# Kernel tuning notes

Hardware: AMD Instinct MI355X
Metric: run time of the kernel (lower is better)

Reference implementation:

```python
import jax, jax.numpy as jnp
import numpy as np

N_U, N_I, E, D = 100000, 50000, 1600000, 128


def setup_inputs() -> dict:
    key = jax.random.key(0)
    ks = jax.random.split(key, 24)
    inp = {
        "x_user": jax.random.normal(ks[0], (N_U, D), jnp.float32),
        "x_item": jax.random.normal(ks[1], (N_I, D), jnp.float32),
        "follows_src": jax.random.randint(ks[2], (E,), 0, N_U, jnp.int32),
        "follows_dst": jax.random.randint(ks[3], (E,), 0, N_U, jnp.int32),
        "rates_src": jax.random.randint(ks[4], (E,), 0, N_U, jnp.int32),
        "rates_dst": jax.random.randint(ks[5], (E,), 0, N_I, jnp.int32),
        "rev_src": jax.random.randint(ks[6], (E,), 0, N_I, jnp.int32),
        "rev_dst": jax.random.randint(ks[7], (E,), 0, N_U, jnp.int32),
    }
    scale = 1.0 / np.sqrt(D)
    wnames = ["W1_follows", "W1_rates", "W1_rev", "W2_follows", "W2_rates", "W2_rev"]
    for i, name in enumerate(wnames):
        inp[name] = jax.random.normal(ks[8 + i], (D, D), jnp.float32) * scale
    bnames = ["b1_follows", "b1_rates", "b1_rev", "b2_follows", "b2_rates", "b2_rev"]
    for i, name in enumerate(bnames):
        inp[name] = jax.random.normal(ks[14 + i], (D,), jnp.float32) * 0.02
    return inp


def _gcn_conv(x_src, src, dst, n_src, n_dst, W, b):
    """Degree-normalized GCN conv on a (possibly bipartite) relation."""
    ones = jnp.ones(src.shape, x_src.dtype)
    deg_s = jax.ops.segment_sum(ones, src, num_segments=n_src)
    deg_d = jax.ops.segment_sum(ones, dst, num_segments=n_dst)
    inv_s = jnp.where(deg_s > 0, 1.0 / jnp.sqrt(deg_s), 0.0)
    inv_d = jnp.where(deg_d > 0, 1.0 / jnp.sqrt(deg_d), 0.0)
    h = x_src @ W                                   # [n_src, out]
    norm = inv_s[src] * inv_d[dst]                  # [E]
    msg = h[src] * norm[:, None]                    # gather + scale
    out = jax.ops.segment_sum(msg, dst, num_segments=n_dst)  # scatter-add
    return out + b


def reference(x_user, x_item, follows_src, follows_dst, rates_src, rates_dst,
              rev_src, rev_dst, W1_follows, b1_follows, W1_rates, b1_rates,
              W1_rev, b1_rev, W2_follows, b2_follows, W2_rates, b2_rates,
              W2_rev, b2_rev):
    # Layer 1: HeteroConv with aggr='mean' over relations sharing dst type
    u = (_gcn_conv(x_user, follows_src, follows_dst, N_U, N_U, W1_follows, b1_follows)
         + _gcn_conv(x_item, rev_src, rev_dst, N_I, N_U, W1_rev, b1_rev)) * 0.5
    it = _gcn_conv(x_user, rates_src, rates_dst, N_U, N_I, W1_rates, b1_rates)
    u = jax.nn.relu(u)
    it = jax.nn.relu(it)
    # Layer 2 (final layer: no relu)
    u2 = (_gcn_conv(u, follows_src, follows_dst, N_U, N_U, W2_follows, b2_follows)
          + _gcn_conv(it, rev_src, rev_dst, N_I, N_U, W2_rev, b2_rev)) * 0.5
    i2 = _gcn_conv(u, rates_src, rates_dst, N_U, N_I, W2_rates, b2_rates)
    # concat node-type outputs into a single array: [N_U + N_I, D]
    return jnp.concatenate([u2, i2], axis=0)
```

## Files before the change

kernel.cpp:

```cpp
#include <hip/hip_runtime.h>
#include <math.h>

static constexpr int NU    = 100000;
static constexpr int NI    = 50000;
static constexpr int NEDGE = 1600000;
static constexpr int DIM   = 128;

__global__ void count_deg_kernel(const int* __restrict__ src, const int* __restrict__ dst,
                                 int* __restrict__ deg_s, int* __restrict__ deg_d, int n) {
  int stride = gridDim.x * blockDim.x;
  for (int i = blockIdx.x * blockDim.x + threadIdx.x; i < n; i += stride) {
    atomicAdd(&deg_s[src[i]], 1);
    atomicAdd(&deg_d[dst[i]], 1);
  }
}

__global__ void inv_sqrt_kernel(int* __restrict__ p, int n) {
  int i = blockIdx.x * blockDim.x + threadIdx.x;
  if (i < n) {
    int v = p[i];
    float f = (v > 0) ? (1.0f / sqrtf((float)v)) : 0.0f;
    p[i] = __float_as_int(f);
  }
}

__global__ __launch_bounds__(1024) void scan_kernel(const int* __restrict__ deg, int n,
                                                    int* __restrict__ rp) {
  __shared__ int wsum[16];
  __shared__ int carry_s;
  const int tid = threadIdx.x, lane = tid & 63, wid = tid >> 6;
  if (tid == 0) carry_s = 0;
  __syncthreads();
  for (int base = 0; base < n; base += 4096) {
    int i0 = base + tid * 4;
    int v0 = 0, v1 = 0, v2 = 0, v3 = 0;
    if (i0 + 3 < n) {
      int4 t = *(const int4*)(deg + i0);
      v0 = t.x; v1 = t.y; v2 = t.z; v3 = t.w;
    } else {
      if (i0     < n) v0 = deg[i0];
      if (i0 + 1 < n) v1 = deg[i0 + 1];
      if (i0 + 2 < n) v2 = deg[i0 + 2];
    }
    int s0 = v0, s1 = s0 + v1, s2 = s1 + v2, s3 = s2 + v3;
    int tot = s3;
    int x = tot;
#pragma unroll
    for (int d2 = 1; d2 < 64; d2 <<= 1) { int y = __shfl_up(x, d2); if (lane >= d2) x += y; }
    if (lane == 63) wsum[wid] = x;
    __syncthreads();
    if (wid == 0) {
      int s = (lane < 16) ? wsum[lane] : 0;
#pragma unroll
      for (int d2 = 1; d2 < 16; d2 <<= 1) { int y = __shfl_up(s, d2); if (lane >= d2) s += y; }
      if (lane < 16) wsum[lane] = s;
    }
    __syncthreads();
    int carry = carry_s;
    int woff = (wid > 0) ? wsum[wid - 1] : 0;
    int base_excl = carry + woff + (x - tot);
    if (i0     < n) rp[i0]     = base_excl;
    if (i0 + 1 < n) rp[i0 + 1] = base_excl + s0;
    if (i0 + 2 < n) rp[i0 + 2] = base_excl + s1;
    if (i0 + 3 < n) rp[i0 + 3] = base_excl + s2;
    __syncthreads();
    if (tid == 0) carry_s = carry + wsum[15];
    __syncthreads();
  }
  if (tid == 0) rp[n] = carry_s;
}

__global__ void fill_kernel(const int* __restrict__ src, const int* __restrict__ dst,
                            const int* __restrict__ rp, int* __restrict__ cnt,
                            int* __restrict__ csr, int n) {
  int stride = gridDim.x * blockDim.x;
  for (int i = blockIdx.x * blockDim.x + threadIdx.x; i < n; i += stride) {
    int d = dst[i];
    int p = atomicAdd(&cnt[d], 1);
    csr[rp[d] + p] = src[i];
  }
}

__global__ __launch_bounds__(256) void gemm128_kernel(const float* __restrict__ A,
                                                      const float* __restrict__ W,
                                                      float* __restrict__ C, int M) {
  __shared__ float As[16][132];
  __shared__ float Bs[16][128];
  const int tid = threadIdx.x;
  const int tx = tid & 15, ty = tid >> 4;
  const int row0 = blockIdx.x * 128;
  float acc[8][8];
#pragma unroll
  for (int r = 0; r < 8; ++r)
#pragma unroll
    for (int c = 0; c < 8; ++c) acc[r][c] = 0.f;

  for (int kk = 0; kk < DIM; kk += 16) {
#pragma unroll
    for (int p = 0; p < 2; ++p) {
      int r = (tid >> 2) + p * 64;
      int kc = (tid & 3) * 4;
      float4 a = make_float4(0.f, 0.f, 0.f, 0.f);
      int row = row0 + r;
      if (row < M) a = *(const float4*)(A + (size_t)row * DIM + kk + kc);
      As[kc + 0][r] = a.x; As[kc + 1][r] = a.y; As[kc + 2][r] = a.z; As[kc + 3][r] = a.w;
    }
    {
      const float4* srcp = (const float4*)(W + kk * DIM);
      float4* dstp = (float4*)(&Bs[0][0]);
      dstp[tid]       = srcp[tid];
      dstp[tid + 256] = srcp[tid + 256];
    }
    __syncthreads();
#pragma unroll
    for (int k = 0; k < 16; ++k) {
      float a[8], b[8];
      *(float4*)&a[0] = *(const float4*)&As[k][ty * 8];
      *(float4*)&a[4] = *(const float4*)&As[k][ty * 8 + 4];
      *(float4*)&b[0] = *(const float4*)&Bs[k][tx * 8];
      *(float4*)&b[4] = *(const float4*)&Bs[k][tx * 8 + 4];
#pragma unroll
      for (int r = 0; r < 8; ++r)
#pragma unroll
        for (int c = 0; c < 8; ++c) acc[r][c] += a[r] * b[c];
    }
    __syncthreads();
  }
#pragma unroll
  for (int r = 0; r < 8; ++r) {
    int row = row0 + ty * 8 + r;
    if (row < M) {
      float4* cp = (float4*)(C + (size_t)row * DIM + tx * 8);
      cp[0] = make_float4(acc[r][0], acc[r][1], acc[r][2], acc[r][3]);
      cp[1] = make_float4(acc[r][4], acc[r][5], acc[r][6], acc[r][7]);
    }
  }
}

template <int MODE, bool RELU>
__global__ __launch_bounds__(256) void agg_kernel(const float* __restrict__ h,
                                                  const int* __restrict__ rp,
                                                  const int* __restrict__ csr,
                                                  const float* __restrict__ inv_s,
                                                  const float* __restrict__ inv_d,
                                                  float* __restrict__ out, int n_dst,
                                                  float scale,
                                                  const float* __restrict__ b1,
                                                  const float* __restrict__ b2) {
  const int lane = threadIdx.x & 63;
  const int row = blockIdx.x * (blockDim.x >> 6) + (threadIdx.x >> 6);
  if (row >= n_dst) return;
  const int e0 = rp[row], e1 = rp[row + 1];
  float ax = 0.f, ay = 0.f;
  for (int base = e0; base < e1; base += 64) {
    const int rem = e1 - base;
    const int m = rem < 64 ? rem : 64;
    int s_l = 0; float w_l = 0.f;
    if (lane < m) { s_l = csr[base + lane]; w_l = inv_s[s_l]; }
    int j = 0;
    for (; j + 3 < m; j += 4) {
      int s0 = __shfl(s_l, j), s1 = __shfl(s_l, j + 1), s2 = __shfl(s_l, j + 2), s3 = __shfl(s_l, j + 3);
      float w0 = __shfl(w_l, j), w1 = __shfl(w_l, j + 1), w2 = __shfl(w_l, j + 2), w3 = __shfl(w_l, j + 3);
      float2 v0 = ((const float2*)(h + (size_t)s0 * DIM))[lane];
      float2 v1 = ((const float2*)(h + (size_t)s1 * DIM))[lane];
      float2 v2 = ((const float2*)(h + (size_t)s2 * DIM))[lane];
      float2 v3 = ((const float2*)(h + (size_t)s3 * DIM))[lane];
      ax += w0 * v0.x + w1 * v1.x + w2 * v2.x + w3 * v3.x;
      ay += w0 * v0.y + w1 * v1.y + w2 * v2.y + w3 * v3.y;
    }
    for (; j < m; ++j) {
      int s0 = __shfl(s_l, j); float w0 = __shfl(w_l, j);
      float2 v0 = ((const float2*)(h + (size_t)s0 * DIM))[lane];
      ax += w0 * v0.x; ay += w0 * v0.y;
    }
  }
  const float invd = inv_d[row];
  float rx = ax * invd, ry = ay * invd;
  float2* op = (float2*)(out + (size_t)row * DIM);
  if (MODE == 0) {
    op[lane] = make_float2(rx, ry);
  } else {
    float bx = 0.f, by = 0.f;
    if (b1) { float2 b = ((const float2*)b1)[lane]; bx += b.x; by += b.y; }
    if (b2) { float2 b = ((const float2*)b2)[lane]; bx += b.x; by += b.y; }
    float px = 0.f, py = 0.f;
    if (MODE == 1) { float2 p = op[lane]; px = p.x; py = p.y; }
    float vx = scale * (px + rx + bx), vy = scale * (py + ry + by);
    if (RELU) { vx = fmaxf(vx, 0.f); vy = fmaxf(vy, 0.f); }
    op[lane] = make_float2(vx, vy);
  }
}

extern "C" void kernel_launch(void* const* d_in, const int* in_sizes, int n_in,
                              void* d_out, int out_size, void* d_ws, size_t ws_size,
                              hipStream_t stream) {
  const float* x_user = (const float*)d_in[0];
  const float* x_item = (const float*)d_in[1];
  const int* f_src = (const int*)d_in[2];
  const int* f_dst = (const int*)d_in[3];
  const int* r_src = (const int*)d_in[4];
  const int* r_dst = (const int*)d_in[5];
  const int* v_src = (const int*)d_in[6];
  const int* v_dst = (const int*)d_in[7];
  const float* W1f = (const float*)d_in[8];
  const float* W1r = (const float*)d_in[9];
  const float* W1v = (const float*)d_in[10];
  const float* W2f = (const float*)d_in[11];
  const float* W2r = (const float*)d_in[12];
  const float* W2v = (const float*)d_in[13];
  const float* b1f = (const float*)d_in[14];
  const float* b1r = (const float*)d_in[15];
  const float* b1v = (const float*)d_in[16];
  const float* b2f = (const float*)d_in[17];
  const float* b2r = (const float*)d_in[18];
  const float* b2v = (const float*)d_in[19];

  char* ws = (char*)d_ws;
  size_t off = 0;
  auto alloc = [&](size_t bytes) {
    size_t o = off;
    off = (off + bytes + 511) & ~(size_t)511;
    return o;
  };
  size_t o_deg = alloc(4ull * (4 * NU + 2 * NI));
  size_t o_rpf = alloc(4ull * (NU + 1));
  size_t o_rpr = alloc(4ull * (NI + 1));
  size_t o_rpv = alloc(4ull * (NU + 1));
  size_t o_cnt = alloc(4ull * (2 * NU + NI));
  size_t o_csf = alloc(4ull * NEDGE);
  size_t o_csr = alloc(4ull * NEDGE);
  size_t o_csv = alloc(4ull * NEDGE);
  size_t o_h   = alloc(4ull * NU * DIM);
  size_t o_u   = alloc(4ull * NU * DIM);
  size_t o_it  = alloc(4ull * NI * DIM);
  (void)ws_size; (void)in_sizes; (void)n_in; (void)out_size;

  int* deg    = (int*)(ws + o_deg);
  int* deg_fs = deg;
  int* deg_fd = deg + NU;
  int* deg_rs = deg + 2 * NU;
  int* deg_rd = deg + 3 * NU;
  int* deg_vs = deg + 3 * NU + NI;
  int* deg_vd = deg + 3 * NU + 2 * NI;

  int* rp_f = (int*)(ws + o_rpf);
  int* rp_r = (int*)(ws + o_rpr);
  int* rp_v = (int*)(ws + o_rpv);
  int* cnt   = (int*)(ws + o_cnt);
  int* cnt_f = cnt;
  int* cnt_r = cnt + NU;
  int* cnt_v = cnt + NU + NI;
  int* csr_f = (int*)(ws + o_csf);
  int* csr_r = (int*)(ws + o_csr);
  int* csr_v = (int*)(ws + o_csv);
  float* h  = (float*)(ws + o_h);
  float* u  = (float*)(ws + o_u);
  float* it = (float*)(ws + o_it);

  float* out_u = (float*)d_out;
  float* out_i = out_u + (size_t)NU * DIM;

  hipMemsetAsync(deg, 0, 4ull * (4 * NU + 2 * NI), stream);
  hipMemsetAsync(cnt, 0, 4ull * (2 * NU + NI), stream);

  count_deg_kernel<<<2048, 256, 0, stream>>>(f_src, f_dst, deg_fs, deg_fd, NEDGE);
  count_deg_kernel<<<2048, 256, 0, stream>>>(r_src, r_dst, deg_rs, deg_rd, NEDGE);
  count_deg_kernel<<<2048, 256, 0, stream>>>(v_src, v_dst, deg_vs, deg_vd, NEDGE);

  scan_kernel<<<1, 1024, 0, stream>>>(deg_fd, NU, rp_f);
  scan_kernel<<<1, 1024, 0, stream>>>(deg_rd, NI, rp_r);
  scan_kernel<<<1, 1024, 0, stream>>>(deg_vd, NU, rp_v);

  inv_sqrt_kernel<<<(4 * NU + 2 * NI + 255) / 256, 256, 0, stream>>>(deg, 4 * NU + 2 * NI);

  fill_kernel<<<2048, 256, 0, stream>>>(f_src, f_dst, rp_f, cnt_f, csr_f, NEDGE);
  fill_kernel<<<2048, 256, 0, stream>>>(r_src, r_dst, rp_r, cnt_r, csr_r, NEDGE);
  fill_kernel<<<2048, 256, 0, stream>>>(v_src, v_dst, rp_v, cnt_v, csr_v, NEDGE);

  const float* inv_fs = (const float*)deg_fs;
  const float* inv_fd = (const float*)deg_fd;
  const float* inv_rs = (const float*)deg_rs;
  const float* inv_rd = (const float*)deg_rd;
  const float* inv_vs = (const float*)deg_vs;
  const float* inv_vd = (const float*)deg_vd;

  gemm128_kernel<<<(NU + 127) / 128, 256, 0, stream>>>(x_user, W1f, h, NU);
  agg_kernel<0, false><<<(NU + 3) / 4, 256, 0, stream>>>(h, rp_f, csr_f, inv_fs, inv_fd,
                                                         u, NU, 1.0f, nullptr, nullptr);
  gemm128_kernel<<<(NI + 127) / 128, 256, 0, stream>>>(x_item, W1v, h, NI);
  agg_kernel<1, true><<<(NU + 3) / 4, 256, 0, stream>>>(h, rp_v, csr_v, inv_vs, inv_vd,
                                                        u, NU, 0.5f, b1f, b1v);
  gemm128_kernel<<<(NU + 127) / 128, 256, 0, stream>>>(x_user, W1r, h, NU);
  agg_kernel<2, true><<<(NI + 3) / 4, 256, 0, stream>>>(h, rp_r, csr_r, inv_rs, inv_rd,
                                                        it, NI, 1.0f, b1r, nullptr);

  gemm128_kernel<<<(NU + 127) / 128, 256, 0, stream>>>(u, W2f, h, NU);
  agg_kernel<0, false><<<(NU + 3) / 4, 256, 0, stream>>>(h, rp_f, csr_f, inv_fs, inv_fd,
                                                         out_u, NU, 1.0f, nullptr, nullptr);
  gemm128_kernel<<<(NI + 127) / 128, 256, 0, stream>>>(it, W2v, h, NI);
  agg_kernel<1, false><<<(NU + 3) / 4, 256, 0, stream>>>(h, rp_v, csr_v, inv_vs, inv_vd,
                                                         out_u, NU, 0.5f, b2f, b2v);
  gemm128_kernel<<<(NU + 127) / 128, 256, 0, stream>>>(u, W2r, h, NU);
  agg_kernel<2, false><<<(NI + 3) / 4, 256, 0, stream>>>(h, rp_r, csr_r, inv_rs, inv_rd,
                                                         out_i, NI, 1.0f, b2r, nullptr);
}
```

Baseline: 2.037 ms.

## Co-schedule independent graph build, GEMMs and aggregations in merged kernels

Degree counting now records each edge's atomic rank, so the CSR fill needs no second atomic counter pass or memset of counters. Independent work (degree counting plus the three layer-1 GEMMs, CSR fills plus the first aggregation, paired aggregations, layer-2 GEMMs plus aggregation) is packed into combined kernels using block-index ranges. This cuts launch count and lets independent stages run concurrently on the GPU. It uses separate h buffers per relation when the workspace is large enough, with a fallback sequential path that reuses buffers otherwise.

```diff
diff --git a/kernel.cpp b/kernel.cpp
--- a/kernel.cpp
+++ b/kernel.cpp
@@ -6,89 +6,57 @@
 static constexpr int NEDGE = 1600000;
 static constexpr int DIM   = 128;
 
-__global__ void count_deg_kernel(const int* __restrict__ src, const int* __restrict__ dst,
-                                 int* __restrict__ deg_s, int* __restrict__ deg_d, int n) {
-  int stride = gridDim.x * blockDim.x;
-  for (int i = blockIdx.x * blockDim.x + threadIdx.x; i < n; i += stride) {
-    atomicAdd(&deg_s[src[i]], 1);
-    atomicAdd(&deg_d[dst[i]], 1);
-  }
-}
-
-__global__ void inv_sqrt_kernel(int* __restrict__ p, int n) {
-  int i = blockIdx.x * blockDim.x + threadIdx.x;
-  if (i < n) {
-    int v = p[i];
-    float f = (v > 0) ? (1.0f / sqrtf((float)v)) : 0.0f;
-    p[i] = __float_as_int(f);
-  }
-}
-
-__global__ __launch_bounds__(1024) void scan_kernel(const int* __restrict__ deg, int n,
-                                                    int* __restrict__ rp) {
-  __shared__ int wsum[16];
-  __shared__ int carry_s;
-  const int tid = threadIdx.x, lane = tid & 63, wid = tid >> 6;
-  if (tid == 0) carry_s = 0;
-  __syncthreads();
-  for (int base = 0; base < n; base += 4096) {
-    int i0 = base + tid * 4;
-    int v0 = 0, v1 = 0, v2 = 0, v3 = 0;
-    if (i0 + 3 < n) {
-      int4 t = *(const int4*)(deg + i0);
-      v0 = t.x; v1 = t.y; v2 = t.z; v3 = t.w;
-    } else {
-      if (i0     < n) v0 = deg[i0];
-      if (i0 + 1 < n) v1 = deg[i0 + 1];
-      if (i0 + 2 < n) v2 = deg[i0 + 2];
-    }
-    int s0 = v0, s1 = s0 + v1, s2 = s1 + v2, s3 = s2 + v3;
-    int tot = s3;
-    int x = tot;
-#pragma unroll
-    for (int d2 = 1; d2 < 64; d2 <<= 1) { int y = __shfl_up(x, d2); if (lane >= d2) x += y; }
-    if (lane == 63) wsum[wid] = x;
-    __syncthreads();
-    if (wid == 0) {
-      int s = (lane < 16) ? wsum[lane] : 0;
-#pragma unroll
-      for (int d2 = 1; d2 < 16; d2 <<= 1) { int y = __shfl_up(s, d2); if (lane >= d2) s += y; }
-      if (lane < 16) wsum[lane] = s;
-    }
-    __syncthreads();
-    int carry = carry_s;
-    int woff = (wid > 0) ? wsum[wid - 1] : 0;
-    int base_excl = carry + woff + (x - tot);
-    if (i0     < n) rp[i0]     = base_excl;
-    if (i0 + 1 < n) rp[i0 + 1] = base_excl + s0;
-    if (i0 + 2 < n) rp[i0 + 2] = base_excl + s1;
-    if (i0 + 3 < n) rp[i0 + 3] = base_excl + s2;
-    __syncthreads();
-    if (tid == 0) carry_s = carry + wsum[15];
-    __syncthreads();
-  }
-  if (tid == 0) rp[n] = carry_s;
-}
-
-__global__ void fill_kernel(const int* __restrict__ src, const int* __restrict__ dst,
-                            const int* __restrict__ rp, int* __restrict__ cnt,
-                            int* __restrict__ csr, int n) {
-  int stride = gridDim.x * blockDim.x;
-  for (int i = blockIdx.x * blockDim.x + threadIdx.x; i < n; i += stride) {
-    int d = dst[i];
-    int p = atomicAdd(&cnt[d], 1);
-    csr[rp[d] + p] = src[i];
-  }
-}
-
-__global__ __launch_bounds__(256) void gemm128_kernel(const float* __restrict__ A,
-                                                      const float* __restrict__ W,
-                                                      float* __restrict__ C, int M) {
-  __shared__ float As[16][132];
-  __shared__ float Bs[16][128];
+static constexpr int CB  = 768;
+static constexpr int GF  = (NU + 127) / 128;
+static constexpr int GV  = (NI + 127) / 128;
+static constexpr int FB  = 512;
+static constexpr int AGU = (NU + 3) / 4;
+static constexpr int AGI = (NI + 3) / 4;
+
+__device__ __forceinline__ void count_rel(const int* __restrict__ src, const int* __restrict__ dst,
+                                          int* __restrict__ deg_s, int* __restrict__ deg_d,
+                                          int* __restrict__ rank, int blk, int nblk) {
+  const int nchunk = NEDGE / 4;
+  const int stride = nblk * 256;
+  for (int c = blk * 256 + threadIdx.x; c < nchunk; c += stride) {
+    int4 s = ((const int4*)src)[c];
+    int4 d = ((const int4*)dst)[c];
+    atomicAdd(&deg_s[s.x], 1);
+    atomicAdd(&deg_s[s.y], 1);
+    atomicAdd(&deg_s[s.z], 1);
+    atomicAdd(&deg_s[s.w], 1);
+    int4 r;
+    r.x = atomicAdd(&deg_d[d.x], 1);
+    r.y = atomicAdd(&deg_d[d.y], 1);
+    r.z = atomicAdd(&deg_d[d.z], 1);
+    r.w = atomicAdd(&deg_d[d.w], 1);
+    ((int4*)rank)[c] = r;
+  }
+}
+
+__device__ __forceinline__ void fill_rel(const int* __restrict__ src, const int* __restrict__ dst,
+                                         const int* __restrict__ rank, const int* __restrict__ rp,
+                                         int* __restrict__ csr, int blk, int nblk) {
+  const int nchunk = NEDGE / 4;
+  const int stride = nblk * 256;
+  for (int c = blk * 256 + threadIdx.x; c < nchunk; c += stride) {
+    int4 s = ((const int4*)src)[c];
+    int4 d = ((const int4*)dst)[c];
+    int4 r = ((const int4*)rank)[c];
+    csr[rp[d.x] + r.x] = s.x;
+    csr[rp[d.y] + r.y] = s.y;
+    csr[rp[d.z] + r.z] = s.z;
+    csr[rp[d.w] + r.w] = s.w;
+  }
+}
+
+__device__ __forceinline__ void gemm_body(const float* __restrict__ A, const float* __restrict__ W,
+                                          float* __restrict__ C, int M, int blk) {
+  static __shared__ float As[16][132];
+  static __shared__ float Bs[16][128];
   const int tid = threadIdx.x;
   const int tx = tid & 15, ty = tid >> 4;
-  const int row0 = blockIdx.x * 128;
+  const int row0 = blk * 128;
   float acc[8][8];
 #pragma unroll
   for (int r = 0; r < 8; ++r)
@@ -138,17 +106,13 @@
 }
 
 template <int MODE, bool RELU>
-__global__ __launch_bounds__(256) void agg_kernel(const float* __restrict__ h,
-                                                  const int* __restrict__ rp,
-                                                  const int* __restrict__ csr,
-                                                  const float* __restrict__ inv_s,
-                                                  const float* __restrict__ inv_d,
-                                                  float* __restrict__ out, int n_dst,
-                                                  float scale,
-                                                  const float* __restrict__ b1,
-                                                  const float* __restrict__ b2) {
+__device__ __forceinline__ void agg_rows(const float* __restrict__ h, const int* __restrict__ rp,
+                                         const int* __restrict__ csr, const float* __restrict__ inv_s,
+                                         const float* __restrict__ inv_d, float* __restrict__ out,
+                                         int n_dst, float scale, const float* __restrict__ b1,
+                                         const float* __restrict__ b2, int blk) {
   const int lane = threadIdx.x & 63;
-  const int row = blockIdx.x * (blockDim.x >> 6) + (threadIdx.x >> 6);
+  const int row = blk * 4 + (threadIdx.x >> 6);
   if (row >= n_dst) return;
   const int e0 = rp[row], e1 = rp[row + 1];
   float ax = 0.f, ay = 0.f;
@@ -189,6 +153,157 @@
     if (RELU) { vx = fmaxf(vx, 0.f); vy = fmaxf(vy, 0.f); }
     op[lane] = make_float2(vx, vy);
   }
+}
+
+__device__ void scan_body(const int* __restrict__ deg, int n, int* __restrict__ rp) {
+  static __shared__ int wsum[16];
+  static __shared__ int carry_s;
+  const int tid = threadIdx.x, lane = tid & 63, wid = tid >> 6;
+  if (tid == 0) carry_s = 0;
+  __syncthreads();
+  for (int base = 0; base < n; base += 4096) {
+    int i0 = base + tid * 4;
+    int v0 = 0, v1 = 0, v2 = 0, v3 = 0;
+    if (i0 + 3 < n) {
+      int4 t = *(const int4*)(deg + i0);
+      v0 = t.x; v1 = t.y; v2 = t.z; v3 = t.w;
+    } else {
+      if (i0     < n) v0 = deg[i0];
+      if (i0 + 1 < n) v1 = deg[i0 + 1];
+      if (i0 + 2 < n) v2 = deg[i0 + 2];
+    }
+    int s0 = v0, s1 = s0 + v1, s2 = s1 + v2, s3 = s2 + v3;
+    int tot = s3;
+    int x = tot;
+#pragma unroll
+    for (int d2 = 1; d2 < 64; d2 <<= 1) { int y = __shfl_up(x, d2); if (lane >= d2) x += y; }
+    if (lane == 63) wsum[wid] = x;
+    __syncthreads();
+    if (wid == 0) {
+      int s = (lane < 16) ? wsum[lane] : 0;
+#pragma unroll
+      for (int d2 = 1; d2 < 16; d2 <<= 1) { int y = __shfl_up(s, d2); if (lane >= d2) s += y; }
+      if (lane < 16) wsum[lane] = s;
+    }
+    __syncthreads();
+    int carry = carry_s;
+    int woff = (wid > 0) ? wsum[wid - 1] : 0;
+    int base_excl = carry + woff + (x - tot);
+    if (i0     < n) rp[i0]     = base_excl;
+    if (i0 + 1 < n) rp[i0 + 1] = base_excl + s0;
+    if (i0 + 2 < n) rp[i0 + 2] = base_excl + s1;
+    if (i0 + 3 < n) rp[i0 + 3] = base_excl + s2;
+    __syncthreads();
+    if (tid == 0) carry_s = carry + wsum[15];
+    __syncthreads();
+  }
+  if (tid == 0) rp[n] = carry_s;
+}
+
+
+__global__ __launch_bounds__(256) void k1_kernel(
+    const int* f_src, const int* f_dst, int* deg_fs, int* deg_fd, int* rank_f,
+    const int* r_src, const int* r_dst, int* deg_rs, int* deg_rd, int* rank_r,
+    const int* v_src, const int* v_dst, int* deg_vs, int* deg_vd, int* rank_v,
+    const float* x_user, const float* x_item,
+    const float* W1f, const float* W1v, const float* W1r,
+    float* h_f, float* h_v, float* h_r) {
+  int b = blockIdx.x;
+  if (b < CB) {
+    count_rel(f_src, f_dst, deg_fs, deg_fd, rank_f, b, CB);
+    count_rel(r_src, r_dst, deg_rs, deg_rd, rank_r, b, CB);
+    count_rel(v_src, v_dst, deg_vs, deg_vd, rank_v, b, CB);
+  } else if (b < CB + GF) {
+    gemm_body(x_user, W1f, h_f, NU, b - CB);
+  } else if (b < CB + GF + GV) {
+    gemm_body(x_item, W1v, h_v, NI, b - CB - GF);
+  } else {
+    gemm_body(x_user, W1r, h_r, NU, b - CB - GF - GV);
+  }
+}
+
+__global__ __launch_bounds__(1024) void scan3_kernel(const int* deg_fd, int* rp_f,
+                                                     const int* deg_rd, int* rp_r,
+                                                     const int* deg_vd, int* rp_v) {
+  if (blockIdx.x == 0)      scan_body(deg_fd, NU, rp_f);
+  else if (blockIdx.x == 1) scan_body(deg_rd, NI, rp_r);
+  else                      scan_body(deg_vd, NU, rp_v);
+}
+
+__global__ void inv_sqrt_kernel(int* __restrict__ p, int n) {
+  int i = blockIdx.x * blockDim.x + threadIdx.x;
+  if (i < n) {
+    int v = p[i];
+    float f = (v > 0) ? (1.0f / sqrtf((float)v)) : 0.0f;
+    p[i] = __float_as_int(f);
+  }
+}
+
+__global__ __launch_bounds__(256) void fill_one_kernel(const int* src, const int* dst,
+                                                       const int* rank, const int* rp, int* csr) {
+  fill_rel(src, dst, rank, rp, csr, blockIdx.x, gridDim.x);
+}
+
+__global__ __launch_bounds__(256) void fill_vr_kernel(
+    const int* v_src, const int* v_dst, const int* rank_v, const int* rp_v, int* csr_v,
+    const int* r_src, const int* r_dst, const int* rank_r, const int* rp_r, int* csr_r) {
+  int b = blockIdx.x;
+  if (b < FB) fill_rel(v_src, v_dst, rank_v, rp_v, csr_v, b, FB);
+  else        fill_rel(r_src, r_dst, rank_r, rp_r, csr_r, b - FB, FB);
+}
+
+__global__ __launch_bounds__(256) void k4_kernel(
+    const int* v_src, const int* v_dst, const int* rank_v, const int* rp_v, int* csr_v,
+    const int* r_src, const int* r_dst, const int* rank_r, const int* rp_r, int* csr_r,
+    const float* h_f, const int* rp_f, const int* csr_f,
+    const float* inv_fs, const float* inv_fd, float* u) {
+  int b = blockIdx.x;
+  if (b < FB)          fill_rel(v_src, v_dst, rank_v, rp_v, csr_v, b, FB);
+  else if (b < 2 * FB) fill_rel(r_src, r_dst, rank_r, rp_r, csr_r, b - FB, FB);
+  else agg_rows<0, false>(h_f, rp_f, csr_f, inv_fs, inv_fd, u, NU, 1.0f, nullptr, nullptr, b - 2 * FB);
+}
+
+__global__ __launch_bounds__(256) void k5_kernel(
+    const float* h_v, const int* rp_v, const int* csr_v, const float* inv_vs, const float* inv_vd,
+    float* u, const float* b1f, const float* b1v,
+    const float* h_r, const int* rp_r, const int* csr_r, const float* inv_rs, const float* inv_rd,
+    float* it, const float* b1r) {
+  int b = blockIdx.x;
+  if (b < AGU) agg_rows<1, true>(h_v, rp_v, csr_v, inv_vs, inv_vd, u, NU, 0.5f, b1f, b1v, b);
+  else         agg_rows<2, true>(h_r, rp_r, csr_r, inv_rs, inv_rd, it, NI, 1.0f, b1r, nullptr, b - AGU);
+}
+
+__global__ __launch_bounds__(256) void gemm_one_kernel(const float* A, const float* W, float* C, int M) {
+  gemm_body(A, W, C, M, blockIdx.x);
+}
+
+__global__ __launch_bounds__(256) void k7_kernel(
+    const float* it, const float* W2v, float* h_v,
+    const float* u,  const float* W2r, float* h_r,
+    const float* h_f, const int* rp_f, const int* csr_f,
+    const float* inv_fs, const float* inv_fd, float* out_u) {
+  int b = blockIdx.x;
+  if (b < GV)           gemm_body(it, W2v, h_v, NI, b);
+  else if (b < GV + GF) gemm_body(u, W2r, h_r, NU, b - GV);
+  else agg_rows<0, false>(h_f, rp_f, csr_f, inv_fs, inv_fd, out_u, NU, 1.0f, nullptr, nullptr, b - GV - GF);
+}
+
+__global__ __launch_bounds__(256) void k8_kernel(
+    const float* h_v, const int* rp_v, const int* csr_v, const float* inv_vs, const float* inv_vd,
+    float* out_u, const float* b2f, const float* b2v,
+    const float* h_r, const int* rp_r, const int* csr_r, const float* inv_rs, const float* inv_rd,
+    float* out_i, const float* b2r) {
+  int b = blockIdx.x;
+  if (b < AGU) agg_rows<1, false>(h_v, rp_v, csr_v, inv_vs, inv_vd, out_u, NU, 0.5f, b2f, b2v, b);
+  else         agg_rows<2, false>(h_r, rp_r, csr_r, inv_rs, inv_rd, out_i, NI, 1.0f, b2r, nullptr, b - AGU);
+}
+
+template <int MODE, bool RELU>
+__global__ __launch_bounds__(256) void agg_kernel(const float* h, const int* rp, const int* csr,
+                                                  const float* inv_s, const float* inv_d,
+                                                  float* out, int n_dst, float scale,
+                                                  const float* b1, const float* b2) {
+  agg_rows<MODE, RELU>(h, rp, csr, inv_s, inv_d, out, n_dst, scale, b1, b2, blockIdx.x);
 }
 
 extern "C" void kernel_launch(void* const* d_in, const int* in_sizes, int n_in,
@@ -214,6 +329,7 @@
   const float* b2f = (const float*)d_in[17];
   const float* b2r = (const float*)d_in[18];
   const float* b2v = (const float*)d_in[19];
+  (void)in_sizes; (void)n_in; (void)out_size;
 
   char* ws = (char*)d_ws;
   size_t off = 0;
@@ -226,14 +342,21 @@
   size_t o_rpf = alloc(4ull * (NU + 1));
   size_t o_rpr = alloc(4ull * (NI + 1));
   size_t o_rpv = alloc(4ull * (NU + 1));
-  size_t o_cnt = alloc(4ull * (2 * NU + NI));
   size_t o_csf = alloc(4ull * NEDGE);
   size_t o_csr = alloc(4ull * NEDGE);
   size_t o_csv = alloc(4ull * NEDGE);
-  size_t o_h   = alloc(4ull * NU * DIM);
+  size_t o_it  = alloc(4ull * NI * DIM);
+  size_t o_hf  = alloc(4ull * NU * DIM);
   size_t o_u   = alloc(4ull * NU * DIM);
-  size_t o_it  = alloc(4ull * NI * DIM);
-  (void)ws_size; (void)in_sizes; (void)n_in; (void)out_size;
+  size_t small_need = off + 512;
+  size_t o_hv  = alloc(4ull * NI * DIM);
+  size_t o_hr  = alloc(4ull * NU * DIM);
+  size_t o_rkf = alloc(4ull * NEDGE);
+  size_t o_rkr = alloc(4ull * NEDGE);
+  size_t o_rkv = alloc(4ull * NEDGE);
+  size_t big_need = off + 512;
+
+  const bool big = (ws_size >= big_need);
 
   int* deg    = (int*)(ws + o_deg);
   int* deg_fs = deg;
@@ -246,36 +369,21 @@
   int* rp_f = (int*)(ws + o_rpf);
   int* rp_r = (int*)(ws + o_rpr);
   int* rp_v = (int*)(ws + o_rpv);
-  int* cnt   = (int*)(ws + o_cnt);
-  int* cnt_f = cnt;
-  int* cnt_r = cnt + NU;
-  int* cnt_v = cnt + NU + NI;
   int* csr_f = (int*)(ws + o_csf);
   int* csr_r = (int*)(ws + o_csr);
   int* csr_v = (int*)(ws + o_csv);
-  float* h  = (float*)(ws + o_h);
-  float* u  = (float*)(ws + o_u);
-  float* it = (float*)(ws + o_it);
+  float* it  = (float*)(ws + o_it);
+  float* h_f = (float*)(ws + o_hf);
+  float* u   = (float*)(ws + o_u);
+  float* h_v = big ? (float*)(ws + o_hv) : h_f;
+  float* h_r = big ? (float*)(ws + o_hr) : h_f;
+  int* rank_f = big ? (int*)(ws + o_rkf) : (int*)(ws + o_u);
+  int* rank_r = big ? (int*)(ws + o_rkr) : (int*)(ws + o_u) + NEDGE;
+  int* rank_v = big ? (int*)(ws + o_rkv) : (int*)(ws + o_u) + 2 * NEDGE;
+  (void)small_need;
 
   float* out_u = (float*)d_out;
   float* out_i = out_u + (size_t)NU * DIM;
-
-  hipMemsetAsync(deg, 0, 4ull * (4 * NU + 2 * NI), stream);
-  hipMemsetAsync(cnt, 0, 4ull * (2 * NU + NI), stream);
-
-  count_deg_kernel<<<2048, 256, 0, stream>>>(f_src, f_dst, deg_fs, deg_fd, NEDGE);
-  count_deg_kernel<<<2048, 256, 0, stream>>>(r_src, r_dst, deg_rs, deg_rd, NEDGE);
-  count_deg_kernel<<<2048, 256, 0, stream>>>(v_src, v_dst, deg_vs, deg_vd, NEDGE);
-
-  scan_kernel<<<1, 1024, 0, stream>>>(deg_fd, NU, rp_f);
-  scan_kernel<<<1, 1024, 0, stream>>>(deg_rd, NI, rp_r);
-  scan_kernel<<<1, 1024, 0, stream>>>(deg_vd, NU, rp_v);
-
-  inv_sqrt_kernel<<<(4 * NU + 2 * NI + 255) / 256, 256, 0, stream>>>(deg, 4 * NU + 2 * NI);
-
-  fill_kernel<<<2048, 256, 0, stream>>>(f_src, f_dst, rp_f, cnt_f, csr_f, NEDGE);
-  fill_kernel<<<2048, 256, 0, stream>>>(r_src, r_dst, rp_r, cnt_r, csr_r, NEDGE);
-  fill_kernel<<<2048, 256, 0, stream>>>(v_src, v_dst, rp_v, cnt_v, csr_v, NEDGE);
 
   const float* inv_fs = (const float*)deg_fs;
   const float* inv_fd = (const float*)deg_fd;
@@ -284,23 +392,54 @@
   const float* inv_vs = (const float*)deg_vs;
   const float* inv_vd = (const float*)deg_vd;
 
-  gemm128_kernel<<<(NU + 127) / 128, 256, 0, stream>>>(x_user, W1f, h, NU);
-  agg_kernel<0, false><<<(NU + 3) / 4, 256, 0, stream>>>(h, rp_f, csr_f, inv_fs, inv_fd,
-                                                         u, NU, 1.0f, nullptr, nullptr);
-  gemm128_kernel<<<(NI + 127) / 128, 256, 0, stream>>>(x_item, W1v, h, NI);
-  agg_kernel<1, true><<<(NU + 3) / 4, 256, 0, stream>>>(h, rp_v, csr_v, inv_vs, inv_vd,
-                                                        u, NU, 0.5f, b1f, b1v);
-  gemm128_kernel<<<(NU + 127) / 128, 256, 0, stream>>>(x_user, W1r, h, NU);
-  agg_kernel<2, true><<<(NI + 3) / 4, 256, 0, stream>>>(h, rp_r, csr_r, inv_rs, inv_rd,
-                                                        it, NI, 1.0f, b1r, nullptr);
-
-  gemm128_kernel<<<(NU + 127) / 128, 256, 0, stream>>>(u, W2f, h, NU);
-  agg_kernel<0, false><<<(NU + 3) / 4, 256, 0, stream>>>(h, rp_f, csr_f, inv_fs, inv_fd,
-                                                         out_u, NU, 1.0f, nullptr, nullptr);
-  gemm128_kernel<<<(NI + 127) / 128, 256, 0, stream>>>(it, W2v, h, NI);
-  agg_kernel<1, false><<<(NU + 3) / 4, 256, 0, stream>>>(h, rp_v, csr_v, inv_vs, inv_vd,
-                                                         out_u, NU, 0.5f, b2f, b2v);
-  gemm128_kernel<<<(NU + 127) / 128, 256, 0, stream>>>(u, W2r, h, NU);
-  agg_kernel<2, false><<<(NI + 3) / 4, 256, 0, stream>>>(h, rp_r, csr_r, inv_rs, inv_rd,
-                                                         out_i, NI, 1.0f, b2r, nullptr);
-}
+  hipMemsetAsync(deg, 0, 4ull * (4 * NU + 2 * NI), stream);
+
+  if (big) {
+    k1_kernel<<<CB + GF + GV + GF, 256, 0, stream>>>(
+        f_src, f_dst, deg_fs, deg_fd, rank_f,
+        r_src, r_dst, deg_rs, deg_rd, rank_r,
+        v_src, v_dst, deg_vs, deg_vd, rank_v,
+        x_user, x_item, W1f, W1v, W1r, h_f, h_v, h_r);
+    scan3_kernel<<<3, 1024, 0, stream>>>(deg_fd, rp_f, deg_rd, rp_r, deg_vd, rp_v);
+    inv_sqrt_kernel<<<(4 * NU + 2 * NI + 1023) / 1024, 1024, 0, stream>>>(deg, 4 * NU + 2 * NI);
+    fill_one_kernel<<<FB, 256, 0, stream>>>(f_src, f_dst, rank_f, rp_f, csr_f);
+    k4_kernel<<<2 * FB + AGU, 256, 0, stream>>>(
+        v_src, v_dst, rank_v, rp_v, csr_v,
+        r_src, r_dst, rank_r, rp_r, csr_r,
+        h_f, rp_f, csr_f, inv_fs, inv_fd, u);
+    k5_kernel<<<AGU + AGI, 256, 0, stream>>>(
+        h_v, rp_v, csr_v, inv_vs, inv_vd, u, b1f, b1v,
+        h_r, rp_r, csr_r, inv_rs, inv_rd, it, b1r);
+    gemm_one_kernel<<<GF, 256, 0, stream>>>(u, W2f, h_f, NU);
+    k7_kernel<<<GV + GF + AGU, 256, 0, stream>>>(
+        it, W2v, h_v, u, W2r, h_r,
+        h_f, rp_f, csr_f, inv_fs, inv_fd, out_u);
+    k8_kernel<<<AGU + AGI, 256, 0, stream>>>(
+        h_v, rp_v, csr_v, inv_vs, inv_vd, out_u, b2f, b2v,
+        h_r, rp_r, csr_r, inv_rs, inv_rd, out_i, b2r);
+  } else {
+    k1_kernel<<<CB, 256, 0, stream>>>(
+        f_src, f_dst, deg_fs, deg_fd, rank_f,
+        r_src, r_dst, deg_rs, deg_rd, rank_r,
+        v_src, v_dst, deg_vs, deg_vd, rank_v,
+        x_user, x_item, W1f, W1v, W1r, h_f, h_v, h_r);
+    scan3_kernel<<<3, 1024, 0, stream>>>(deg_fd, rp_f, deg_rd, rp_r, deg_vd, rp_v);
+    inv_sqrt_kernel<<<(4 * NU + 2 * NI + 1023) / 1024, 1024, 0, stream>>>(deg, 4 * NU + 2 * NI);
+    fill_one_kernel<<<FB, 256, 0, stream>>>(f_src, f_dst, rank_f, rp_f, csr_f);
+    fill_vr_kernel<<<2 * FB, 256, 0, stream>>>(
+        v_src, v_dst, rank_v, rp_v, csr_v,
+        r_src, r_dst, rank_r, rp_r, csr_r);
+    gemm_one_kernel<<<GF, 256, 0, stream>>>(x_user, W1f, h_f, NU);
+    agg_kernel<0, false><<<AGU, 256, 0, stream>>>(h_f, rp_f, csr_f, inv_fs, inv_fd, u, NU, 1.0f, nullptr, nullptr);
+    gemm_one_kernel<<<GV, 256, 0, stream>>>(x_item, W1v, h_f, NI);
+    agg_kernel<1, true><<<AGU, 256, 0, stream>>>(h_f, rp_v, csr_v, inv_vs, inv_vd, u, NU, 0.5f, b1f, b1v);
+    gemm_one_kernel<<<GF, 256, 0, stream>>>(x_user, W1r, h_f, NU);
+    agg_kernel<2, true><<<AGI, 256, 0, stream>>>(h_f, rp_r, csr_r, inv_rs, inv_rd, it, NI, 1.0f, b1r, nullptr);
+    gemm_one_kernel<<<GF, 256, 0, stream>>>(u, W2f, h_f, NU);
+    agg_kernel<0, false><<<AGU, 256, 0, stream>>>(h_f, rp_f, csr_f, inv_fs, inv_fd, out_u, NU, 1.0f, nullptr, nullptr);
+    gemm_one_kernel<<<GV, 256, 0, stream>>>(it, W2v, h_f, NI);
+    agg_kernel<1, false><<<AGU, 256, 0, stream>>>(h_f, rp_v, csr_v, inv_vs, inv_vd, out_u, NU, 0.5f, b2f, b2v);
+    gemm_one_kernel<<<GF, 256, 0, stream>>>(u, W2r, h_f, NU);
+    agg_kernel<2, false><<<AGI, 256, 0, stream>>>(h_f, rp_r, csr_r, inv_rs, inv_rd, out_i, NI, 1.0f, b2r, nullptr);
+  }
+}
```

Result: faster. 1.945 ms (-4.5%).
